# Optimization experiments

Measured on AMD Instinct MI355X. Metric: run time of the kernel, lower is better.

## Reference

```python
import jax, jax.numpy as jnp
import numpy as np

B_BATCH = 2048
D = 1024
L_CACHE = 3
N_LAYERS = 12
LAYER_IDX = 0


def setup_inputs() -> dict:
    key = jax.random.key(0)
    ks = jax.random.split(key, 5)
    x = jax.random.normal(ks[0], (B_BATCH, 1, D), dtype=jnp.float32)
    conv_cache = jax.random.normal(ks[1], (N_LAYERS, B_BATCH, D, L_CACHE), dtype=jnp.float32)
    cache_position = jnp.ones((1,), dtype=jnp.int64 if jax.config.jax_enable_x64 else jnp.int32)
    in_proj_w = jax.random.normal(ks[2], (3 * D, D), dtype=jnp.float32) * 0.02
    out_proj_w = jax.random.normal(ks[3], (D, D), dtype=jnp.float32) * 0.02
    conv_w = jax.random.normal(ks[4], (D, 1, L_CACHE), dtype=jnp.float32) * 0.2
    return {"x": x, "conv_cache": conv_cache, "cache_position": cache_position,
            "in_proj_w": in_proj_w, "out_proj_w": out_proj_w, "conv_w": conv_w}


def reference(x, conv_cache, cache_position, in_proj_w, out_proj_w, conv_w):
    # x: [B, 1, D] decode step. attention_mask path is a no-op for seq_len==1.
    # in_proj then transpose(-1,-2): [B, 3D, 1]
    BCx = jnp.swapaxes(jnp.einsum('bld,ed->ble', x, in_proj_w), -1, -2)
    Bg, Cg, xg = jnp.split(BCx, 3, axis=-2)  # each [B, D, 1]
    Bx = Bg * xg  # gate; feeds (discarded) cache update in the original

    # WithCache branch (cache_position[0] > 0):
    conv_state = conv_cache[LAYER_IDX]  # [B, D, L_cache]
    # Original computes new_conv_state = roll + indexed write of Bx, but it is
    # discarded; conv_out uses the OLD conv_state. Faithfully reproduced:
    # new_conv_state = jnp.roll(conv_state, -1, axis=-1).at[:, :, jnp.clip(cache_position, 0, L_CACHE-1)].set(Bx)
    conv_out = jnp.sum(conv_state * conv_w[:, 0, :], axis=-1)[..., None]  # [B, D, 1]

    y = Cg * conv_out                      # [B, D, 1]
    y = jnp.swapaxes(y, -1, -2)            # [B, 1, D]
    return jnp.einsum('bld,ed->ble', y, out_proj_w)
```

## Files before the change

### kernel.cpp

```cpp
#include <hip/hip_runtime.h>
#include <hip/hip_bf16.h>


#define BDIM 2048
#define DDIM 1024

typedef __attribute__((ext_vector_type(8))) short bf16x8;
typedef __attribute__((ext_vector_type(4))) float f32x4;

__device__ __forceinline__ unsigned short bf16rn(float f) {
    unsigned int u = __builtin_bit_cast(unsigned int, f);
    return (unsigned short)((u + 0x7FFFu + ((u >> 16) & 1u)) >> 16);
}

#define GLDS16(gp, lp)                                                          \
    __builtin_amdgcn_global_load_lds(                                           \
        (const __attribute__((address_space(1))) void*)(gp),                    \
        (__attribute__((address_space(3))) void*)(lp), 16, 0, 0)

__global__ __launch_bounds__(256) void prep_cast(
    const float* __restrict__ x, const float* __restrict__ w1,
    const float* __restrict__ w2, unsigned short* __restrict__ xb,
    unsigned short* __restrict__ w1b, unsigned short* __restrict__ w2b)
{
    const int t = blockIdx.x * 256 + threadIdx.x;
    const int X4 = BDIM * DDIM / 4;
    const int W4 = DDIM * DDIM / 4;
    float4 v;
    unsigned short* dst;
    if (t < X4) {
        v = ((const float4*)x)[t];
        dst = xb + (size_t)t * 4;
    } else if (t < X4 + W4) {
        int u = t - X4;
        v = ((const float4*)(w1 + (size_t)DDIM * DDIM))[u];
        dst = w1b + (size_t)u * 4;
    } else {
        int u = t - X4 - W4;
        v = ((const float4*)w2)[u];
        dst = w2b + (size_t)u * 4;
    }
    ushort4 o;
    o.x = bf16rn(v.x); o.y = bf16rn(v.y); o.z = bf16rn(v.z); o.w = bf16rn(v.w);
    *(ushort4*)dst = o;
}

template <bool GATE>
__global__ __launch_bounds__(64) void gemm64(
    const unsigned short* __restrict__ A, const unsigned short* __restrict__ B,
    const float* __restrict__ cache,
    const float* __restrict__ convw,
    unsigned short* __restrict__ Ybf, float* __restrict__ Yf32, int K)
{
    __shared__ unsigned short ldsA[64 * 32];
    __shared__ unsigned short ldsB[64 * 32];

    const int lane = threadIdx.x;
    const int col  = lane & 15;
    const int quad = lane >> 4;
    const int m0   = blockIdx.y * 64;
    const int n0   = blockIdx.x * 64;

    const int rsub = lane >> 2;
    const int kel  = (lane & 3) * 8;
    const unsigned short* aSrc[4];
    const unsigned short* bSrc[4];
#pragma unroll
    for (int t = 0; t < 4; ++t) {
        aSrc[t] = A + (size_t)(m0 + t * 16 + rsub) * K + kel;
        bSrc[t] = B + (size_t)(n0 + t * 16 + rsub) * K + kel;
    }

    f32x4 acc[4][4] = {};

    for (int k0 = 0; k0 < K; k0 += 32) {
#pragma unroll
        for (int t = 0; t < 4; ++t) GLDS16(aSrc[t] + k0, &ldsA[t * 512]);
#pragma unroll
        for (int t = 0; t < 4; ++t) GLDS16(bSrc[t] + k0, &ldsB[t * 512]);
        __syncthreads();

        bf16x8 av[4], bv[4];
#pragma unroll
        for (int i = 0; i < 4; ++i)
            av[i] = *(const bf16x8*)&ldsA[(i * 16 + col) * 32 + quad * 8];
#pragma unroll
        for (int j = 0; j < 4; ++j)
            bv[j] = *(const bf16x8*)&ldsB[(j * 16 + col) * 32 + quad * 8];
#pragma unroll
        for (int i = 0; i < 4; ++i)
#pragma unroll
            for (int j = 0; j < 4; ++j)
                acc[i][j] = __builtin_amdgcn_mfma_f32_16x16x32_bf16(
                    av[i], bv[j], acc[i][j], 0, 0, 0);
        __syncthreads();
    }

#pragma unroll
    for (int j = 0; j < 4; ++j) {
        const int n = n0 + j * 16 + col;
        float cw0, cw1, cw2;
        if (GATE) {
            cw0 = convw[n * 3 + 0];
            cw1 = convw[n * 3 + 1];
            cw2 = convw[n * 3 + 2];
        }
#pragma unroll
        for (int i = 0; i < 4; ++i) {
#pragma unroll
            for (int r = 0; r < 4; ++r) {
                const int m = m0 + i * 16 + quad * 4 + r;
                const float v = acc[i][j][r];
                if (GATE) {
                    const float* cp = cache + ((size_t)m * DDIM + n) * 3;
                    const float co = cp[0] * cw0 + cp[1] * cw1 + cp[2] * cw2;
                    Ybf[(size_t)m * DDIM + n] = bf16rn(v * co);
                } else {
                    Yf32[(size_t)m * DDIM + n] = v;
                }
            }
        }
    }
}

extern "C" void kernel_launch(void* const* d_in, const int* in_sizes, int n_in,
                              void* d_out, int out_size, void* d_ws, size_t ws_size,
                              hipStream_t stream)
{
    const float* x     = (const float*)d_in[0];
    const float* cache = (const float*)d_in[1];
    const float* w1    = (const float*)d_in[3];
    const float* w2    = (const float*)d_in[4];
    const float* cw    = (const float*)d_in[5];
    float* out = (float*)d_out;

    unsigned short* xb  = (unsigned short*)d_ws;
    unsigned short* w1b = xb  + (size_t)BDIM * DDIM;
    unsigned short* w2b = w1b + (size_t)DDIM * DDIM;
    unsigned short* yb  = w2b + (size_t)DDIM * DDIM;

    prep_cast<<<dim3(4096), dim3(256), 0, stream>>>(x, w1, w2, xb, w1b, w2b);

    dim3 grid(DDIM / 64, BDIM / 64);
    gemm64<true><<<grid, dim3(64), 0, stream>>>(xb, w1b, cache, cw, yb, nullptr, DDIM);
    gemm64<false><<<grid, dim3(64), 0, stream>>>(yb, w2b, nullptr, nullptr, nullptr, out, DDIM);
}
```

Measured before the change: 395.1 us.

## Use two-wave blocks, K-step 64, and XOR-swizzled LDS in GEMM

New measurement: 377.5 us. 4.5% less time.

```diff
diff --git a/kernel.cpp b/kernel.cpp
--- a/kernel.cpp
+++ b/kernel.cpp
@@ -2,8 +2,9 @@
 #include <hip/hip_bf16.h>
 
 
-#define BDIM 2048
-#define DDIM 1024
+#define MDIM 2048
+#define NDIM 1024
+#define KDIM 1024
 
 typedef __attribute__((ext_vector_type(8))) short bf16x8;
 typedef __attribute__((ext_vector_type(4))) float f32x4;
@@ -24,8 +25,8 @@
     unsigned short* __restrict__ w1b, unsigned short* __restrict__ w2b)
 {
     const int t = blockIdx.x * 256 + threadIdx.x;
-    const int X4 = BDIM * DDIM / 4;
-    const int W4 = DDIM * DDIM / 4;
+    const int X4 = MDIM * KDIM / 4;
+    const int W4 = KDIM * NDIM / 4;
     float4 v;
     unsigned short* dst;
     if (t < X4) {
@@ -33,7 +34,7 @@
         dst = xb + (size_t)t * 4;
     } else if (t < X4 + W4) {
         int u = t - X4;
-        v = ((const float4*)(w1 + (size_t)DDIM * DDIM))[u];
+        v = ((const float4*)(w1 + (size_t)NDIM * KDIM))[u];
         dst = w1b + (size_t)u * 4;
     } else {
         int u = t - X4 - W4;
@@ -46,59 +47,67 @@
 }
 
 template <bool GATE>
-__global__ __launch_bounds__(64) void gemm64(
-    const unsigned short* __restrict__ A, const unsigned short* __restrict__ B,
+__global__ __launch_bounds__(128) void gemm(
+    const unsigned short* __restrict__ A, const unsigned short* __restrict__ Bm,
     const float* __restrict__ cache,
     const float* __restrict__ convw,
-    unsigned short* __restrict__ Ybf, float* __restrict__ Yf32, int K)
+    unsigned short* __restrict__ Ybf, float* __restrict__ Yout)
 {
-    __shared__ unsigned short ldsA[64 * 32];
-    __shared__ unsigned short ldsB[64 * 32];
+    __shared__ unsigned short ldsA[64 * 64];
+    __shared__ unsigned short ldsB[64 * 64];
 
-    const int lane = threadIdx.x;
+    const int tid  = threadIdx.x;
+    const int lane = tid & 63;
+    const int w    = tid >> 6;
     const int col  = lane & 15;
     const int quad = lane >> 4;
     const int m0   = blockIdx.y * 64;
     const int n0   = blockIdx.x * 64;
 
-    const int rsub = lane >> 2;
-    const int kel  = (lane & 3) * 8;
-    const unsigned short* aSrc[4];
-    const unsigned short* bSrc[4];
+    const int rsub = lane >> 3;
+    const int kg   = (lane & 7) ^ rsub;
+    size_t aoff[4], boff[4];
 #pragma unroll
     for (int t = 0; t < 4; ++t) {
-        aSrc[t] = A + (size_t)(m0 + t * 16 + rsub) * K + kel;
-        bSrc[t] = B + (size_t)(n0 + t * 16 + rsub) * K + kel;
+        const int c = 4 * w + t;
+        aoff[t] = (size_t)(m0 + 8 * c + rsub) * KDIM + kg * 8;
+        boff[t] = (size_t)(n0 + 8 * c + rsub) * KDIM + kg * 8;
     }
 
-    f32x4 acc[4][4] = {};
+    f32x4 acc[4][2] = {};
 
-    for (int k0 = 0; k0 < K; k0 += 32) {
+    for (int k0 = 0; k0 < KDIM; k0 += 64) {
 #pragma unroll
-        for (int t = 0; t < 4; ++t) GLDS16(aSrc[t] + k0, &ldsA[t * 512]);
-#pragma unroll
-        for (int t = 0; t < 4; ++t) GLDS16(bSrc[t] + k0, &ldsB[t * 512]);
+        for (int t = 0; t < 4; ++t) {
+            const int c = 4 * w + t;
+            GLDS16(A + aoff[t] + k0, &ldsA[c * 512]);
+            GLDS16(Bm + boff[t] + k0, &ldsB[c * 512]);
+        }
         __syncthreads();
 
-        bf16x8 av[4], bv[4];
 #pragma unroll
-        for (int i = 0; i < 4; ++i)
-            av[i] = *(const bf16x8*)&ldsA[(i * 16 + col) * 32 + quad * 8];
+        for (int ks = 0; ks < 2; ++ks) {
+            const int slot = (ks * 4 + quad) ^ (col & 7);
+            bf16x8 av[4], bv[2];
 #pragma unroll
-        for (int j = 0; j < 4; ++j)
-            bv[j] = *(const bf16x8*)&ldsB[(j * 16 + col) * 32 + quad * 8];
+            for (int i = 0; i < 4; ++i)
+                av[i] = *(const bf16x8*)&ldsA[(i * 16 + col) * 64 + slot * 8];
 #pragma unroll
-        for (int i = 0; i < 4; ++i)
+            for (int j = 0; j < 2; ++j)
+                bv[j] = *(const bf16x8*)&ldsB[(w * 32 + j * 16 + col) * 64 + slot * 8];
 #pragma unroll
-            for (int j = 0; j < 4; ++j)
-                acc[i][j] = __builtin_amdgcn_mfma_f32_16x16x32_bf16(
-                    av[i], bv[j], acc[i][j], 0, 0, 0);
+            for (int i = 0; i < 4; ++i)
+#pragma unroll
+                for (int j = 0; j < 2; ++j)
+                    acc[i][j] = __builtin_amdgcn_mfma_f32_16x16x32_bf16(
+                        av[i], bv[j], acc[i][j], 0, 0, 0);
+        }
         __syncthreads();
     }
 
 #pragma unroll
-    for (int j = 0; j < 4; ++j) {
-        const int n = n0 + j * 16 + col;
+    for (int j = 0; j < 2; ++j) {
+        const int n = n0 + w * 32 + j * 16 + col;
         float cw0, cw1, cw2;
         if (GATE) {
             cw0 = convw[n * 3 + 0];
@@ -110,13 +119,13 @@
 #pragma unroll
             for (int r = 0; r < 4; ++r) {
                 const int m = m0 + i * 16 + quad * 4 + r;
-                const float v = acc[i][j][r];
+                float v = acc[i][j][r];
                 if (GATE) {
-                    const float* cp = cache + ((size_t)m * DDIM + n) * 3;
-                    const float co = cp[0] * cw0 + cp[1] * cw1 + cp[2] * cw2;
-                    Ybf[(size_t)m * DDIM + n] = bf16rn(v * co);
+                    const float* cp = cache + ((size_t)m * NDIM + n) * 3;
+                    v *= cp[0] * cw0 + cp[1] * cw1 + cp[2] * cw2;
+                    Ybf[(size_t)m * NDIM + n] = bf16rn(v);
                 } else {
-                    Yf32[(size_t)m * DDIM + n] = v;
+                    Yout[(size_t)m * NDIM + n] = v;
                 }
             }
         }
@@ -135,13 +144,13 @@
     float* out = (float*)d_out;
 
     unsigned short* xb  = (unsigned short*)d_ws;
-    unsigned short* w1b = xb  + (size_t)BDIM * DDIM;
-    unsigned short* w2b = w1b + (size_t)DDIM * DDIM;
-    unsigned short* yb  = w2b + (size_t)DDIM * DDIM;
+    unsigned short* w1b = xb  + (size_t)MDIM * KDIM;
+    unsigned short* w2b = w1b + (size_t)KDIM * NDIM;
+    unsigned short* yb  = w2b + (size_t)KDIM * NDIM;
 
     prep_cast<<<dim3(4096), dim3(256), 0, stream>>>(x, w1, w2, xb, w1b, w2b);
 
-    dim3 grid(DDIM / 64, BDIM / 64);
-    gemm64<true><<<grid, dim3(64), 0, stream>>>(xb, w1b, cache, cw, yb, nullptr, DDIM);
-    gemm64<false><<<grid, dim3(64), 0, stream>>>(yb, w2b, nullptr, nullptr, nullptr, out, DDIM);
+    dim3 grid(NDIM / 64, MDIM / 64);
+    gemm<true><<<grid, dim3(128), 0, stream>>>(xb, w1b, cache, cw, yb, nullptr);
+    gemm<false><<<grid, dim3(128), 0, stream>>>(yb, w2b, nullptr, nullptr, nullptr, out);
 }
```
